# Kernel tuning notes

Hardware: AMD Instinct MI355X
Metric: run time of the kernel (lower is better)

The kernel has to match this reference:

```python
import jax, jax.numpy as jnp
import numpy as np

BN_EPS = 1e-5

def _bn_eval(x, gamma, beta):
    # Fresh torch BatchNorm1d in eval mode: running_mean=0, running_var=1
    return x * (gamma / jnp.sqrt(1.0 + BN_EPS)) + beta

def setup_inputs() -> dict:
    key = jax.random.key(0)
    ks = jax.random.split(key, 10)
    Q, K, H, W, D = 64, 128, 24, 8, 128
    L = H * W            # seq_len = 192
    FF = 2048            # dim_feedforward
    q_feat = jax.random.normal(ks[0], (Q, H, W, D), dtype=jnp.float32)
    g_feat = jax.random.normal(ks[1], (K, H, W, D), dtype=jnp.float32)
    se = jax.random.normal(ks[2], (L, L), dtype=jnp.float32)
    score_embed = (se + se.T).reshape(1, 1, L, L)
    s = 1.0 / np.sqrt(D)
    fc0_w = jax.random.uniform(ks[3], (D, D), jnp.float32, -s, s)
    fc0_b = jax.random.uniform(ks[4], (D,), jnp.float32, -s, s)
    s2 = 1.0 / np.sqrt(L)
    fc2_w = jax.random.uniform(ks[5], (FF, L), jnp.float32, -s2, s2)
    fc2_b = jax.random.uniform(ks[6], (FF,), jnp.float32, -s2, s2)
    s3 = 1.0 / np.sqrt(FF)
    fc3_w = jax.random.uniform(ks[7], (1, FF), jnp.float32, -s3, s3)
    fc3_b = jax.random.uniform(ks[8], (1,), jnp.float32, -s3, s3)
    bn1_g = jnp.ones((1,)); bn1_b = jnp.zeros((1,))
    bn2_g = jnp.ones((FF,)) + 0.1 * jax.random.normal(ks[9], (FF,), jnp.float32)
    bn2_b = jnp.zeros((FF,))
    bn3_g = jnp.ones((1,)); bn3_b = jnp.zeros((1,))
    return dict(q_feat=q_feat, g_feat=g_feat, score_embed=score_embed,
                fc0_w=fc0_w, fc0_b=fc0_b, fc2_w=fc2_w, fc2_b=fc2_b,
                fc3_w=fc3_w, fc3_b=fc3_b, bn1_g=bn1_g, bn1_b=bn1_b,
                bn2_g=bn2_g, bn2_b=bn2_b, bn3_g=bn3_g, bn3_b=bn3_b)

def reference(q_feat, g_feat, score_embed, fc0_w, fc0_b, fc2_w, fc2_b,
              fc3_w, fc3_b, bn1_g, bn1_b, bn2_g, bn2_b, bn3_g, bn3_b):
    Q = q_feat.shape[0]
    K = g_feat.shape[0]
    D = q_feat.shape[-1]
    L = score_embed.shape[-1]  # seq_len
    tgt = q_feat.reshape(Q, L, D)
    mem = g_feat.reshape(K, L, D)
    query = tgt @ fc0_w.T + fc0_b      # [Q, L, D]
    key_ = mem @ fc0_w.T + fc0_b       # [K, L, D]
    # [Q, K, L(s), L(t)] score, modulated by broadcast sigmoid bias
    score = jnp.einsum('qtd,ksd->qkst', query, key_) * jax.nn.sigmoid(score_embed)
    score = score.reshape(Q * K, L, L)
    # max over s and over t, concatenated per pair -> [QK, 2L]
    score = jnp.concatenate([score.max(axis=1), score.max(axis=2)], axis=-1)
    score = score.reshape(-1, L)       # [2*QK, L]
    score = _bn_eval(score, bn1_g, bn1_b)
    score = score @ fc2_w.T + fc2_b    # [2*QK, FF]
    score = _bn_eval(score, bn2_g, bn2_b)
    score = jax.nn.relu(score)
    score = score @ fc3_w.T + fc3_b    # [2*QK, 1]
    score = score.reshape(-1, 2).sum(axis=-1, keepdims=True)  # [QK, 1]
    score = _bn_eval(score, bn3_g, bn3_b)
    return score.reshape(Q, K)
```

## Files before the change

kernel.cpp:

```cpp
#include <hip/hip_runtime.h>
#include <hip/hip_fp16.h>

#define LL 192
#define FF 2048

typedef __attribute__((__ext_vector_type__(8)))  __bf16 bf16x8;
typedef __attribute__((__ext_vector_type__(4)))  __bf16 bf16x4;
typedef __attribute__((__ext_vector_type__(4)))  float  f32x4;
typedef __attribute__((__ext_vector_type__(2)))  _Float16 f16x2;

#define MFMA16(a, b, c) __builtin_amdgcn_mfma_f32_16x16x32_bf16((a), (b), (c), 0, 0, 0)


template<int CTL>
__device__ __forceinline__ unsigned dppu(unsigned x) {
    return (unsigned)__builtin_amdgcn_mov_dpp((int)x, CTL, 0xF, 0xF, true);
}
__device__ __forceinline__ unsigned pkrtz_u(float a, float b) {
    return __builtin_bit_cast(unsigned, __builtin_amdgcn_cvt_pkrtz(a, b));
}
__device__ __forceinline__ unsigned hmax2u(unsigned a, unsigned b) {
    unsigned r;
    asm("v_pk_max_f16 %0, %1, %2" : "=v"(r) : "v"(a), "v"(b));
    return r;
}

__launch_bounds__(256, 2)
__global__ void proj_prep_kernel(const float* __restrict__ qf_in,
                                 const float* __restrict__ gf_in,
                                 const float* __restrict__ fc0w,
                                 const float* __restrict__ fc0b,
                                 const float* __restrict__ se,
                                 const float* __restrict__ fc2w,
                                 const float* __restrict__ fc2b,
                                 const float* __restrict__ bn2g,
                                 const float* __restrict__ bn2b,
                                 const float* __restrict__ fc3w,
                                 __bf16* __restrict__ kfragA,
                                 __bf16* __restrict__ qfrag16,
                                 float* __restrict__ sig32,
                                 __bf16* __restrict__ fc2w_bf,
                                 float* __restrict__ h2,
                                 float* __restrict__ bb2,
                                 float* __restrict__ f3)
{
    int bx = blockIdx.x, tid = threadIdx.x;
    if (bx >= 1152) {
        int i0 = (bx - 1152) * 256 + tid;
        const int stride = 160 * 256;
        const float c1 = rsqrtf(1.f + 1e-5f);
        for (int i = i0; i < LL * LL; i += stride) {
            int r = i & 3, lane = (i >> 2) & 63, tile = i >> 8;
            int jt = tile % 12, st = tile / 12;
            int s = st * 16 + (lane >> 4) * 4 + r;
            int t = jt * 16 + (lane & 15);
            sig32[i] = 1.f / (1.f + __expf(-se[s * 192 + t]));
        }
        for (int i = i0; i < FF * LL; i += stride)
            fc2w_bf[i] = (__bf16)fc2w[i];
        for (int i = i0; i < FF; i += stride) {
            float h = bn2g[i] * c1;
            h2[i]  = h;
            bb2[i] = fc2b[i] * h + bn2b[i];
            f3[i]  = fc3w[i];
        }
        return;
    }
    __shared__ __bf16 Xs[32][136];
    __shared__ __bf16 Ws[128][136];
    __shared__ __bf16 Os[4096];
    const float* src = (bx < 384) ? (qf_in + (size_t)bx * (32 * 128))
                                  : (gf_in + (size_t)(bx - 384) * (32 * 128));
#pragma unroll
    for (int it = 0; it < 4; ++it) {
        int e = (it * 256 + tid) * 4;
        int r = e >> 7, c = e & 127;
        float4 v = *reinterpret_cast<const float4*>(src + e);
        bf16x4 xv;
        xv[0] = (__bf16)v.x; xv[1] = (__bf16)v.y;
        xv[2] = (__bf16)v.z; xv[3] = (__bf16)v.w;
        *reinterpret_cast<bf16x4*>(&Xs[r][c]) = xv;
    }
#pragma unroll
    for (int it = 0; it < 16; ++it) {
        int e = (it * 256 + tid) * 4;
        int r = e >> 7, c = e & 127;
        float4 v = *reinterpret_cast<const float4*>(fc0w + e);
        bf16x4 xv;
        xv[0] = (__bf16)v.x; xv[1] = (__bf16)v.y;
        xv[2] = (__bf16)v.z; xv[3] = (__bf16)v.w;
        *reinterpret_cast<bf16x4*>(&Ws[r][c]) = xv;
    }
    __syncthreads();

    int wv = tid >> 6, lane = tid & 63, quad = lane >> 4, l16 = lane & 15;
    int n0 = wv * 32;
    f32x4 acc[2][2];
#pragma unroll
    for (int m = 0; m < 2; ++m)
#pragma unroll
        for (int n = 0; n < 2; ++n) acc[m][n] = (f32x4){0.f, 0.f, 0.f, 0.f};
#pragma unroll
    for (int ks = 0; ks < 4; ++ks) {
        bf16x8 a0 = *reinterpret_cast<const bf16x8*>(&Xs[l16][ks * 32 + quad * 8]);
        bf16x8 a1 = *reinterpret_cast<const bf16x8*>(&Xs[16 + l16][ks * 32 + quad * 8]);
        bf16x8 b0 = *reinterpret_cast<const bf16x8*>(&Ws[n0 + l16][ks * 32 + quad * 8]);
        bf16x8 b1 = *reinterpret_cast<const bf16x8*>(&Ws[n0 + 16 + l16][ks * 32 + quad * 8]);
        acc[0][0] = MFMA16(a0, b0, acc[0][0]);
        acc[0][1] = MFMA16(a0, b1, acc[0][1]);
        acc[1][0] = MFMA16(a1, b0, acc[1][0]);
        acc[1][1] = MFMA16(a1, b1, acc[1][1]);
    }
#pragma unroll
    for (int mt = 0; mt < 2; ++mt)
#pragma unroll
        for (int nt = 0; nt < 2; ++nt) {
            int d = n0 + nt * 16 + l16;
            float bv = fc0b[d];
            int abase = mt * 2048 + (d >> 5) * 512 + ((d >> 3) & 3) * 128 + (d & 7);
#pragma unroll
            for (int r = 0; r < 4; ++r)
                Os[abase + (quad * 4 + r) * 8] = (__bf16)(acc[mt][nt][r] + bv);
        }
    __syncthreads();

    int row0 = bx * 32;
    __bf16* dst;
    if (bx < 384) {
        int qi = row0 / 192, tg0 = (row0 % 192) >> 4;
        dst = qfrag16 + qi * 24576 + tg0 * 2048;
    } else {
        int rk0 = row0 - 12288;
        int ki = rk0 / 192, sg0 = (rk0 % 192) >> 4;
        dst = kfragA + ki * 24576 + sg0 * 2048;
    }
#pragma unroll
    for (int it = 0; it < 2; ++it) {
        int e = (it * 256 + tid) * 8;
        *reinterpret_cast<bf16x8*>(dst + e) =
            *reinterpret_cast<const bf16x8*>(&Os[e]);
    }
}

__launch_bounds__(256, 2)
__global__ void score_kernel(const __bf16* __restrict__ kfragA,
                             const __bf16* __restrict__ qfrag16,
                             const float* __restrict__ sig32,
                             const float* __restrict__ bn1g,
                             const float* __restrict__ bn1b,
                             __bf16* __restrict__ Sred)
{
    __shared__ unsigned rowP[2][16][98];

    int tid = threadIdx.x;
    int q0 = (blockIdx.x & 31) * 2;
    int kbase = (blockIdx.x >> 5) << 2;
    int w = tid >> 6, lane = tid & 63, quad = lane >> 4, l16 = lane & 15;
    const float g1c = bn1g[0] * rsqrtf(1.f + 1e-5f);
    const float b1v = bn1b[0];
    const float* sigb = sig32 + 768 * w + 4 * lane;

    bf16x8 Bf[2][3][4];
#pragma unroll
    for (int p = 0; p < 2; ++p) {
        const __bf16* qb = qfrag16 + (size_t)(q0 + p) * 24576 + lane * 8;
#pragma unroll
        for (int j = 0; j < 3; ++j)
#pragma unroll
            for (int ks = 0; ks < 4; ++ks)
                Bf[p][j][ks] = *reinterpret_cast<const bf16x8*>(
                    qb + ((3 * w + j) * 4 + ks) * 512);
    }

#pragma unroll 1
    for (int kk = 0; kk < 4; ++kk) {
        int kidx = kbase + kk;
        const __bf16* ka = kfragA + (size_t)kidx * 24576 + lane * 8;
        float cm[2][3];
#pragma unroll
        for (int p = 0; p < 2; ++p)
#pragma unroll
            for (int j = 0; j < 3; ++j) cm[p][j] = -3.0e38f;

#pragma unroll 1
        for (int sc = 0; sc < 6; ++sc) {
            f32x4 acc[2][2][3];

#pragma unroll
            for (int ks = 0; ks < 4; ++ks) {
                bf16x8 a0 = *reinterpret_cast<const bf16x8*>(
                    ka + (sc * 2 + 0) * 2048 + ks * 512);
                bf16x8 a1 = *reinterpret_cast<const bf16x8*>(
                    ka + (sc * 2 + 1) * 2048 + ks * 512);
                if (ks == 0) {
                    const f32x4 Z4 = (f32x4){0.f, 0.f, 0.f, 0.f};
#pragma unroll
                    for (int j = 0; j < 3; ++j) {
                        acc[0][0][j] = MFMA16(a0, Bf[0][j][0], Z4);
                        acc[0][1][j] = MFMA16(a1, Bf[0][j][0], Z4);
                        acc[1][0][j] = MFMA16(a0, Bf[1][j][0], Z4);
                        acc[1][1][j] = MFMA16(a1, Bf[1][j][0], Z4);
                    }
                } else {
#pragma unroll
                    for (int j = 0; j < 3; ++j) {
                        acc[0][0][j] = MFMA16(a0, Bf[0][j][ks], acc[0][0][j]);
                        acc[0][1][j] = MFMA16(a1, Bf[0][j][ks], acc[0][1][j]);
                        acc[1][0][j] = MFMA16(a0, Bf[1][j][ks], acc[1][0][j]);
                        acc[1][1][j] = MFMA16(a1, Bf[1][j][ks], acc[1][1][j]);
                    }
                }
            }

#pragma unroll
            for (int i = 0; i < 2; ++i) {
                int stile = sc * 2 + i;
                const float* sp = sigb + stile * 3072;
                f32x4 s0 = *reinterpret_cast<const f32x4*>(sp);
                f32x4 s1 = *reinterpret_cast<const f32x4*>(sp + 256);
                f32x4 s2 = *reinterpret_cast<const f32x4*>(sp + 512);
#pragma unroll
                for (int p = 0; p < 2; ++p) {
                    f32x4 v0 = acc[p][i][0] * s0;
                    f32x4 v1 = acc[p][i][1] * s1;
                    f32x4 v2 = acc[p][i][2] * s2;
                    cm[p][0] = fmaxf(fmaxf(cm[p][0], fmaxf(v0[0], v0[1])),
                                     fmaxf(v0[2], v0[3]));
                    cm[p][1] = fmaxf(fmaxf(cm[p][1], fmaxf(v1[0], v1[1])),
                                     fmaxf(v1[2], v1[3]));
                    cm[p][2] = fmaxf(fmaxf(cm[p][2], fmaxf(v2[0], v2[1])),
                                     fmaxf(v2[2], v2[3]));
                    unsigned h01 = pkrtz_u(
                        fmaxf(fmaxf(v0[0], v1[0]), v2[0]),
                        fmaxf(fmaxf(v0[1], v1[1]), v2[1]));
                    unsigned h23 = pkrtz_u(
                        fmaxf(fmaxf(v0[2], v1[2]), v2[2]),
                        fmaxf(fmaxf(v0[3], v1[3]), v2[3]));
                    h01 = hmax2u(h01, dppu<0xB1>(h01));
                    h01 = hmax2u(h01, dppu<0x4E>(h01));
                    h23 = hmax2u(h23, dppu<0xB1>(h23));
                    h23 = hmax2u(h23, dppu<0x4E>(h23));
                    if ((l16 & 3) == 0) {
                        int rp = stile * 8 + quad * 2;
                        rowP[p][(l16 >> 2) * 4 + w][rp]     = h01;
                        rowP[p][(l16 >> 2) * 4 + w][rp + 1] = h23;
                    }
                }
            }
        }

#pragma unroll
        for (int p = 0; p < 2; ++p) {
            size_t ob = (size_t)((q0 + p) * 128 + kidx) * 384;
            float v0 = cm[p][0], v1 = cm[p][1], v2 = cm[p][2];
            v0 = fmaxf(v0, __shfl_xor(v0, 16, 64));
            v0 = fmaxf(v0, __shfl_xor(v0, 32, 64));
            v1 = fmaxf(v1, __shfl_xor(v1, 16, 64));
            v1 = fmaxf(v1, __shfl_xor(v1, 32, 64));
            v2 = fmaxf(v2, __shfl_xor(v2, 16, 64));
            v2 = fmaxf(v2, __shfl_xor(v2, 32, 64));
            if (quad == 0) {
                Sred[ob + (3 * w + 0) * 16 + l16] = (__bf16)(v0 * g1c + b1v);
                Sred[ob + (3 * w + 1) * 16 + l16] = (__bf16)(v1 * g1c + b1v);
                Sred[ob + (3 * w + 2) * 16 + l16] = (__bf16)(v2 * g1c + b1v);
            }
        }

        __syncthreads();

        if (tid < 96) {
#pragma unroll
            for (int p = 0; p < 2; ++p) {
                size_t ob = (size_t)((q0 + p) * 128 + kidx) * 384;
                unsigned m = rowP[p][0][tid];
#pragma unroll
                for (int c = 1; c < 16; ++c)
                    m = hmax2u(m, rowP[p][c][tid]);
                __half2 hm = __builtin_bit_cast(__half2, m);
                float lo = __low2float(hm), hi = __high2float(hm);
                unsigned two =
                    (unsigned)__builtin_bit_cast(unsigned short,
                        (__bf16)(lo * g1c + b1v)) |
                    ((unsigned)__builtin_bit_cast(unsigned short,
                        (__bf16)(hi * g1c + b1v)) << 16);
                *reinterpret_cast<unsigned*>(&Sred[ob + 192 + 2 * tid]) = two;
            }
        }

        __syncthreads();
    }
}

__launch_bounds__(512, 1)
__global__ void mlp_kernel(const __bf16* __restrict__ Sred,
                           const __bf16* __restrict__ fc2w_bf,
                           const float* __restrict__ h2,
                           const float* __restrict__ bb2,
                           const float* __restrict__ f3,
                           const float* __restrict__ fc3b,
                           const float* __restrict__ bn3g,
                           const float* __restrict__ bn3b,
                           float* __restrict__ out)
{
    __shared__ __bf16 As[64][200];
    __shared__ float  psum_lds[8][64];
    int bx = blockIdx.x, tid = threadIdx.x;
    const __bf16* asrc = Sred + (size_t)bx * (64 * 192);
#pragma unroll
    for (int it = 0; it < 3; ++it) {
        int e = (it * 512 + tid) * 8;
        int r = e / 192, c = e - r * 192;
        *reinterpret_cast<bf16x8*>(&As[r][c]) =
            *reinterpret_cast<const bf16x8*>(asrc + e);
    }
    __syncthreads();

    int wv = tid >> 6, lane = tid & 63, quad = lane >> 4, l16 = lane & 15;
    bf16x8 af[4][6];
#pragma unroll
    for (int m = 0; m < 4; ++m)
#pragma unroll
        for (int kk = 0; kk < 6; ++kk)
            af[m][kk] = *reinterpret_cast<const bf16x8*>(
                &As[m * 16 + l16][kk * 32 + quad * 8]);

    float ps[4][4] = {{0.f,0.f,0.f,0.f},{0.f,0.f,0.f,0.f},
                      {0.f,0.f,0.f,0.f},{0.f,0.f,0.f,0.f}};
    for (int nt = 0; nt < 16; ++nt) {
        int n0 = wv * 256 + nt * 16;
        f32x4 acc[4];
#pragma unroll
        for (int m = 0; m < 4; ++m) acc[m] = (f32x4){0.f, 0.f, 0.f, 0.f};
        const __bf16* bp = fc2w_bf + (size_t)(n0 + l16) * 192 + quad * 8;
#pragma unroll
        for (int kk = 0; kk < 6; ++kk) {
            bf16x8 b = *reinterpret_cast<const bf16x8*>(bp + kk * 32);
#pragma unroll
            for (int m = 0; m < 4; ++m) acc[m] = MFMA16(af[m][kk], b, acc[m]);
        }
        int n = n0 + l16;
        float hh = h2[n], bb = bb2[n], ffv = f3[n];
#pragma unroll
        for (int m = 0; m < 4; ++m)
#pragma unroll
            for (int r = 0; r < 4; ++r)
                ps[m][r] += fmaxf(acc[m][r] * hh + bb, 0.f) * ffv;
    }
#pragma unroll
    for (int m = 0; m < 4; ++m)
#pragma unroll
        for (int r = 0; r < 4; ++r) {
            float v = ps[m][r];
            v += __shfl_xor(v, 1, 64);
            v += __shfl_xor(v, 2, 64);
            v += __shfl_xor(v, 4, 64);
            v += __shfl_xor(v, 8, 64);
            if (l16 == 0) psum_lds[wv][m * 16 + quad * 4 + r] = v;
        }
    __syncthreads();
    if (tid < 32) {
        float s = 0.f;
#pragma unroll
        for (int w = 0; w < 8; ++w)
            s += psum_lds[w][2 * tid] + psum_lds[w][2 * tid + 1];
        const float c1 = rsqrtf(1.f + 1e-5f);
        out[bx * 32 + tid] = (s + 2.f * fc3b[0]) * (bn3g[0] * c1) + bn3b[0];
    }
}

extern "C" void kernel_launch(void* const* d_in, const int* in_sizes, int n_in,
                              void* d_out, int out_size, void* d_ws, size_t ws_size,
                              hipStream_t stream)
{
    const float* q_feat = (const float*)d_in[0];
    const float* g_feat = (const float*)d_in[1];
    const float* se     = (const float*)d_in[2];
    const float* fc0w   = (const float*)d_in[3];
    const float* fc0b   = (const float*)d_in[4];
    const float* fc2w   = (const float*)d_in[5];
    const float* fc2b   = (const float*)d_in[6];
    const float* fc3w   = (const float*)d_in[7];
    const float* fc3b   = (const float*)d_in[8];
    const float* bn1g   = (const float*)d_in[9];
    const float* bn1b   = (const float*)d_in[10];
    const float* bn2g   = (const float*)d_in[11];
    const float* bn2b   = (const float*)d_in[12];
    const float* bn3g   = (const float*)d_in[13];
    const float* bn3b   = (const float*)d_in[14];
    float* out = (float*)d_out;

    char* ws = (char*)d_ws;
    __bf16* kfragA   = (__bf16*)(ws);
    __bf16* qfrag16  = (__bf16*)(ws +  6291456);
    float*  sig32    = (float*) (ws +  9437184);
    __bf16* fc2w_bf  = (__bf16*)(ws +  9584640);
    float*  h2       = (float*) (ws + 10371072);
    float*  bb2      = (float*) (ws + 10379264);
    float*  f3       = (float*) (ws + 10387456);
    __bf16* Sred     = (__bf16*)(ws + 10395648);

    proj_prep_kernel<<<1312, 256, 0, stream>>>(q_feat, g_feat, fc0w, fc0b, se,
                                               fc2w, fc2b, bn2g, bn2b, fc3w,
                                               kfragA, qfrag16, sig32, fc2w_bf,
                                               h2, bb2, f3);
    score_kernel<<<1024, 256, 0, stream>>>(kfragA, qfrag16, sig32, bn1g, bn1b, Sred);
    mlp_kernel<<<256, 512, 0, stream>>>(Sred, fc2w_bf, h2, bb2, f3,
                                        fc3b, bn3g, bn3b, out);
}
```

Measured before the change: 223.0 us.

## Software-pipeline score kernel MFMA with epilogue, one query per block

Each score_kernel block now handles a single query instead of two, which doubles the grid to 2048 blocks and halves the register footprint of the B fragments and accumulators. The s-tile loop becomes a software pipeline with ping-pong A fragments and accumulators. The MFMA for the next tile and the A prefetch are issued before the max/reduction epilogue of the current tile, with sched_barrier enforcing that order. This is meant to hide global-load and MFMA latency behind epilogue ALU work, at the cost of reloading each key's A fragments twice as often across blocks.

```diff
diff --git a/kernel.cpp b/kernel.cpp
--- a/kernel.cpp
+++ b/kernel.cpp
@@ -142,6 +142,55 @@
     }
 }
 
+__device__ __forceinline__ void load_a(bf16x8 (&a)[4], const __bf16* ka, int t) {
+#pragma unroll
+    for (int ks = 0; ks < 4; ++ks)
+        a[ks] = *reinterpret_cast<const bf16x8*>(ka + t * 2048 + ks * 512);
+}
+
+__device__ __forceinline__ void load_sig(f32x4 (&s)[3], const float* sigb, int st) {
+    const float* sp = sigb + st * 3072;
+    s[0] = *reinterpret_cast<const f32x4*>(sp);
+    s[1] = *reinterpret_cast<const f32x4*>(sp + 256);
+    s[2] = *reinterpret_cast<const f32x4*>(sp + 512);
+}
+
+__device__ __forceinline__ void mfma_tile(f32x4 (&acc)[3], const bf16x8 (&a)[4],
+                                          const bf16x8 (&Bf)[3][4]) {
+    const f32x4 Z4 = (f32x4){0.f, 0.f, 0.f, 0.f};
+#pragma unroll
+    for (int j = 0; j < 3; ++j) acc[j] = MFMA16(a[0], Bf[j][0], Z4);
+#pragma unroll
+    for (int ks = 1; ks < 4; ++ks)
+#pragma unroll
+        for (int j = 0; j < 3; ++j) acc[j] = MFMA16(a[ks], Bf[j][ks], acc[j]);
+}
+
+__device__ __forceinline__ void epi_tile(const f32x4 (&acc)[3], const f32x4 (&s)[3],
+                                         float (&cm)[3], int st,
+                                         int quad, int l16, int w,
+                                         unsigned (*rowP)[98]) {
+    f32x4 v0 = acc[0] * s[0];
+    f32x4 v1 = acc[1] * s[1];
+    f32x4 v2 = acc[2] * s[2];
+    cm[0] = fmaxf(fmaxf(cm[0], fmaxf(v0[0], v0[1])), fmaxf(v0[2], v0[3]));
+    cm[1] = fmaxf(fmaxf(cm[1], fmaxf(v1[0], v1[1])), fmaxf(v1[2], v1[3]));
+    cm[2] = fmaxf(fmaxf(cm[2], fmaxf(v2[0], v2[1])), fmaxf(v2[2], v2[3]));
+    unsigned h01 = pkrtz_u(fmaxf(fmaxf(v0[0], v1[0]), v2[0]),
+                           fmaxf(fmaxf(v0[1], v1[1]), v2[1]));
+    unsigned h23 = pkrtz_u(fmaxf(fmaxf(v0[2], v1[2]), v2[2]),
+                           fmaxf(fmaxf(v0[3], v1[3]), v2[3]));
+    h01 = hmax2u(h01, dppu<0xB1>(h01));
+    h01 = hmax2u(h01, dppu<0x4E>(h01));
+    h23 = hmax2u(h23, dppu<0xB1>(h23));
+    h23 = hmax2u(h23, dppu<0x4E>(h23));
+    if ((l16 & 3) == 0) {
+        int rp = st * 8 + quad * 2;
+        rowP[(l16 >> 2) * 4 + w][rp]     = h01;
+        rowP[(l16 >> 2) * 4 + w][rp + 1] = h23;
+    }
+}
+
 __launch_bounds__(256, 2)
 __global__ void score_kernel(const __bf16* __restrict__ kfragA,
                              const __bf16* __restrict__ qfrag16,
@@ -150,25 +199,24 @@
                              const float* __restrict__ bn1b,
                              __bf16* __restrict__ Sred)
 {
-    __shared__ unsigned rowP[2][16][98];
+    __shared__ unsigned rowP[16][98];
 
     int tid = threadIdx.x;
-    int q0 = (blockIdx.x & 31) * 2;
-    int kbase = (blockIdx.x >> 5) << 2;
+    int q0 = blockIdx.x & 63;
+    int kbase = (blockIdx.x >> 6) << 2;
     int w = tid >> 6, lane = tid & 63, quad = lane >> 4, l16 = lane & 15;
     const float g1c = bn1g[0] * rsqrtf(1.f + 1e-5f);
     const float b1v = bn1b[0];
     const float* sigb = sig32 + 768 * w + 4 * lane;
 
-    bf16x8 Bf[2][3][4];
-#pragma unroll
-    for (int p = 0; p < 2; ++p) {
-        const __bf16* qb = qfrag16 + (size_t)(q0 + p) * 24576 + lane * 8;
+    bf16x8 Bf[3][4];
+    {
+        const __bf16* qb = qfrag16 + (size_t)q0 * 24576 + lane * 8;
 #pragma unroll
         for (int j = 0; j < 3; ++j)
 #pragma unroll
             for (int ks = 0; ks < 4; ++ks)
-                Bf[p][j][ks] = *reinterpret_cast<const bf16x8*>(
+                Bf[j][ks] = *reinterpret_cast<const bf16x8*>(
                     qb + ((3 * w + j) * 4 + ks) * 512);
     }
 
@@ -176,83 +224,41 @@
     for (int kk = 0; kk < 4; ++kk) {
         int kidx = kbase + kk;
         const __bf16* ka = kfragA + (size_t)kidx * 24576 + lane * 8;
-        float cm[2][3];
-#pragma unroll
-        for (int p = 0; p < 2; ++p)
-#pragma unroll
-            for (int j = 0; j < 3; ++j) cm[p][j] = -3.0e38f;
-
-#pragma unroll 1
-        for (int sc = 0; sc < 6; ++sc) {
-            f32x4 acc[2][2][3];
-
-#pragma unroll
-            for (int ks = 0; ks < 4; ++ks) {
-                bf16x8 a0 = *reinterpret_cast<const bf16x8*>(
-                    ka + (sc * 2 + 0) * 2048 + ks * 512);
-                bf16x8 a1 = *reinterpret_cast<const bf16x8*>(
-                    ka + (sc * 2 + 1) * 2048 + ks * 512);
-                if (ks == 0) {
-                    const f32x4 Z4 = (f32x4){0.f, 0.f, 0.f, 0.f};
-#pragma unroll
-                    for (int j = 0; j < 3; ++j) {
-                        acc[0][0][j] = MFMA16(a0, Bf[0][j][0], Z4);
-                        acc[0][1][j] = MFMA16(a1, Bf[0][j][0], Z4);
-                        acc[1][0][j] = MFMA16(a0, Bf[1][j][0], Z4);
-                        acc[1][1][j] = MFMA16(a1, Bf[1][j][0], Z4);
-                    }
-                } else {
-#pragma unroll
-                    for (int j = 0; j < 3; ++j) {
-                        acc[0][0][j] = MFMA16(a0, Bf[0][j][ks], acc[0][0][j]);
-                        acc[0][1][j] = MFMA16(a1, Bf[0][j][ks], acc[0][1][j]);
-                        acc[1][0][j] = MFMA16(a0, Bf[1][j][ks], acc[1][0][j]);
-                        acc[1][1][j] = MFMA16(a1, Bf[1][j][ks], acc[1][1][j]);
-                    }
-                }
-            }
-
-#pragma unroll
-            for (int i = 0; i < 2; ++i) {
-                int stile = sc * 2 + i;
-                const float* sp = sigb + stile * 3072;
-                f32x4 s0 = *reinterpret_cast<const f32x4*>(sp);
-                f32x4 s1 = *reinterpret_cast<const f32x4*>(sp + 256);
-                f32x4 s2 = *reinterpret_cast<const f32x4*>(sp + 512);
-#pragma unroll
-                for (int p = 0; p < 2; ++p) {
-                    f32x4 v0 = acc[p][i][0] * s0;
-                    f32x4 v1 = acc[p][i][1] * s1;
-                    f32x4 v2 = acc[p][i][2] * s2;
-                    cm[p][0] = fmaxf(fmaxf(cm[p][0], fmaxf(v0[0], v0[1])),
-                                     fmaxf(v0[2], v0[3]));
-                    cm[p][1] = fmaxf(fmaxf(cm[p][1], fmaxf(v1[0], v1[1])),
-                                     fmaxf(v1[2], v1[3]));
-                    cm[p][2] = fmaxf(fmaxf(cm[p][2], fmaxf(v2[0], v2[1])),
-                                     fmaxf(v2[2], v2[3]));
-                    unsigned h01 = pkrtz_u(
-                        fmaxf(fmaxf(v0[0], v1[0]), v2[0]),
-                        fmaxf(fmaxf(v0[1], v1[1]), v2[1]));
-                    unsigned h23 = pkrtz_u(
-                        fmaxf(fmaxf(v0[2], v1[2]), v2[2]),
-                        fmaxf(fmaxf(v0[3], v1[3]), v2[3]));
-                    h01 = hmax2u(h01, dppu<0xB1>(h01));
-                    h01 = hmax2u(h01, dppu<0x4E>(h01));
-                    h23 = hmax2u(h23, dppu<0xB1>(h23));
-                    h23 = hmax2u(h23, dppu<0x4E>(h23));
-                    if ((l16 & 3) == 0) {
-                        int rp = stile * 8 + quad * 2;
-                        rowP[p][(l16 >> 2) * 4 + w][rp]     = h01;
-                        rowP[p][(l16 >> 2) * 4 + w][rp + 1] = h23;
-                    }
-                }
-            }
-        }
-
-#pragma unroll
-        for (int p = 0; p < 2; ++p) {
-            size_t ob = (size_t)((q0 + p) * 128 + kidx) * 384;
-            float v0 = cm[p][0], v1 = cm[p][1], v2 = cm[p][2];
+        float cm[3] = {-3.0e38f, -3.0e38f, -3.0e38f};
+
+        bf16x8 aA[4], aB[4];
+        f32x4 accA[3], accB[3];
+        f32x4 sv[3];
+
+        load_a(aA, ka, 0);
+        load_a(aB, ka, 1);
+        mfma_tile(accA, aA, Bf);
+        load_a(aA, ka, 2);
+
+#pragma unroll
+        for (int st = 0; st < 10; st += 2) {
+            load_sig(sv, sigb, st);
+            mfma_tile(accB, aB, Bf);
+            load_a(aB, ka, st + 3);
+            __builtin_amdgcn_sched_barrier(0);
+            epi_tile(accA, sv, cm, st, quad, l16, w, rowP);
+
+            load_sig(sv, sigb, st + 1);
+            mfma_tile(accA, aA, Bf);
+            load_a(aA, ka, (st + 4 > 11) ? 11 : st + 4);
+            __builtin_amdgcn_sched_barrier(0);
+            epi_tile(accB, sv, cm, st + 1, quad, l16, w, rowP);
+        }
+        load_sig(sv, sigb, 10);
+        mfma_tile(accB, aB, Bf);
+        __builtin_amdgcn_sched_barrier(0);
+        epi_tile(accA, sv, cm, 10, quad, l16, w, rowP);
+        load_sig(sv, sigb, 11);
+        epi_tile(accB, sv, cm, 11, quad, l16, w, rowP);
+
+        {
+            size_t ob = (size_t)(q0 * 128 + kidx) * 384;
+            float v0 = cm[0], v1 = cm[1], v2 = cm[2];
             v0 = fmaxf(v0, __shfl_xor(v0, 16, 64));
             v0 = fmaxf(v0, __shfl_xor(v0, 32, 64));
             v1 = fmaxf(v1, __shfl_xor(v1, 16, 64));
@@ -269,22 +275,19 @@
         __syncthreads();
 
         if (tid < 96) {
-#pragma unroll
-            for (int p = 0; p < 2; ++p) {
-                size_t ob = (size_t)((q0 + p) * 128 + kidx) * 384;
-                unsigned m = rowP[p][0][tid];
-#pragma unroll
-                for (int c = 1; c < 16; ++c)
-                    m = hmax2u(m, rowP[p][c][tid]);
-                __half2 hm = __builtin_bit_cast(__half2, m);
-                float lo = __low2float(hm), hi = __high2float(hm);
-                unsigned two =
-                    (unsigned)__builtin_bit_cast(unsigned short,
-                        (__bf16)(lo * g1c + b1v)) |
-                    ((unsigned)__builtin_bit_cast(unsigned short,
-                        (__bf16)(hi * g1c + b1v)) << 16);
-                *reinterpret_cast<unsigned*>(&Sred[ob + 192 + 2 * tid]) = two;
-            }
+            size_t ob = (size_t)(q0 * 128 + kidx) * 384;
+            unsigned m = rowP[0][tid];
+#pragma unroll
+            for (int c = 1; c < 16; ++c)
+                m = hmax2u(m, rowP[c][tid]);
+            __half2 hm = __builtin_bit_cast(__half2, m);
+            float lo = __low2float(hm), hi = __high2float(hm);
+            unsigned two =
+                (unsigned)__builtin_bit_cast(unsigned short,
+                    (__bf16)(lo * g1c + b1v)) |
+                ((unsigned)__builtin_bit_cast(unsigned short,
+                    (__bf16)(hi * g1c + b1v)) << 16);
+            *reinterpret_cast<unsigned*>(&Sred[ob + 192 + 2 * tid]) = two;
         }
 
         __syncthreads();
@@ -403,7 +406,7 @@
                                                fc2w, fc2b, bn2g, bn2b, fc3w,
                                                kfragA, qfrag16, sig32, fc2w_bf,
                                                h2, bb2, f3);
-    score_kernel<<<1024, 256, 0, stream>>>(kfragA, qfrag16, sig32, bn1g, bn1b, Sred);
+    score_kernel<<<2048, 256, 0, stream>>>(kfragA, qfrag16, sig32, bn1g, bn1b, Sred);
     mlp_kernel<<<256, 512, 0, stream>>>(Sred, fc2w_bf, h2, bb2, f3,
                                         fc3b, bn3g, bn3b, out);
 }
```

After: 296.0 us. 32.7% more time.
